# Kernel optimization log

Measured on AMD Instinct MI355X. Metric: run time of the kernel, lower is better.

The kernel has to match this reference:

```python
import jax, jax.numpy as jnp
import numpy as np


def setup_inputs() -> dict:
    key = jax.random.key(0)
    k1, k2, k3, k4 = jax.random.split(key, 4)
    B = 50000    # batch nodes (len(neighbor_lists))
    E = 800000   # total neighbor edges (avg degree 16)
    N = 100000   # unique neighbor embedding rows
    D = 96       # feature dim
    embedding = jax.random.normal(k1, (B * 0 + N, D), dtype=jnp.float32)
    self_feats = jax.random.normal(k2, (B, D), dtype=jnp.float32)
    neighbor_idx = jax.random.randint(k3, (E,), 0, N, dtype=jnp.int64)
    seg_ids = jnp.sort(jax.random.randint(k4, (E,), 0, B, dtype=jnp.int64))
    return {
        "embedding": embedding,
        "self_feats": self_feats,
        "neighbor_idx": neighbor_idx,
        "seg_ids": seg_ids,
    }


def reference(embedding, self_feats, neighbor_idx, seg_ids):
    # Segment-mean aggregation: equivalent to the original's row-normalized
    # dense mask matmul mask.mm(embedding[neighbors_new_index]), but without
    # materializing the [B, n_unique] mask.
    B = self_feats.shape[0]
    gathered = embedding[neighbor_idx]                          # [E, D]
    sums = jax.ops.segment_sum(gathered, seg_ids, num_segments=B)   # [B, D]
    counts = jax.ops.segment_sum(
        jnp.ones(seg_ids.shape, dtype=embedding.dtype), seg_ids, num_segments=B
    )                                                            # [B]
    # every batch node has >=1 neighbor in the original; guard div-by-zero
    feats_1 = sums / jnp.maximum(counts, 1)[:, None]             # neighbor mean
    feats_2 = self_feats - feats_1
    return jnp.concatenate([feats_1, feats_2], axis=1)          # [B, 2D]
```

## Files before the change

### kernel.cpp

```cpp
#include <hip/hip_runtime.h>
#include <stdint.h>

#define DIMS 96
#define VEC 4
#define LANES (DIMS / VEC)
#define SEGS_PER_BLOCK 16
#define THREADS (LANES * SEGS_PER_BLOCK)

__global__ __launch_bounds__(THREADS) void seg_mean_concat_kernel(
    const float* __restrict__ emb,
    const float* __restrict__ self_feats,
    const int*   __restrict__ nidx,
    const int*   __restrict__ seg,
    float* __restrict__ out,
    int B, int E)
{
    __shared__ int bounds[SEGS_PER_BLOCK + 1];

    const int b0 = blockIdx.x * SEGS_PER_BLOCK;
    const int tid = threadIdx.x;

    if (tid <= SEGS_PER_BLOCK) {
        const int v = b0 + tid;
        int lo = 0, hi = E;
        while (lo < hi) {
            int mid = (lo + hi) >> 1;
            if (seg[mid] < v) lo = mid + 1; else hi = mid;
        }
        bounds[tid] = lo;
    }
    __syncthreads();

    const int g    = tid / LANES;
    const int lane = tid - g * LANES;
    const int b    = b0 + g;
    if (b >= B) return;

    const int start = bounds[g];
    const int end   = bounds[g + 1];

    const float4* __restrict__ embv = (const float4*)emb;

    float4 acc = make_float4(0.f, 0.f, 0.f, 0.f);

    int e = start;
    for (; e + 8 <= end; e += 8) {
        const int j0 = nidx[e + 0];
        const int j1 = nidx[e + 1];
        const int j2 = nidx[e + 2];
        const int j3 = nidx[e + 3];
        const int j4 = nidx[e + 4];
        const int j5 = nidx[e + 5];
        const int j6 = nidx[e + 6];
        const int j7 = nidx[e + 7];
        const float4 v0 = embv[(size_t)j0 * LANES + lane];
        const float4 v1 = embv[(size_t)j1 * LANES + lane];
        const float4 v2 = embv[(size_t)j2 * LANES + lane];
        const float4 v3 = embv[(size_t)j3 * LANES + lane];
        const float4 v4 = embv[(size_t)j4 * LANES + lane];
        const float4 v5 = embv[(size_t)j5 * LANES + lane];
        const float4 v6 = embv[(size_t)j6 * LANES + lane];
        const float4 v7 = embv[(size_t)j7 * LANES + lane];
        acc.x += v0.x + v1.x + v2.x + v3.x + v4.x + v5.x + v6.x + v7.x;
        acc.y += v0.y + v1.y + v2.y + v3.y + v4.y + v5.y + v6.y + v7.y;
        acc.z += v0.z + v1.z + v2.z + v3.z + v4.z + v5.z + v6.z + v7.z;
        acc.w += v0.w + v1.w + v2.w + v3.w + v4.w + v5.w + v6.w + v7.w;
    }
    for (; e < end; ++e) {
        const int j = nidx[e];
        const float4 v = embv[(size_t)j * LANES + lane];
        acc.x += v.x; acc.y += v.y; acc.z += v.z; acc.w += v.w;
    }

    const int cnt = end - start;
    const float inv = 1.0f / (float)(cnt > 0 ? cnt : 1);
    float4 mean;
    mean.x = acc.x * inv; mean.y = acc.y * inv;
    mean.z = acc.z * inv; mean.w = acc.w * inv;

    const float4 sf = *(const float4*)(self_feats + (size_t)b * DIMS + lane * VEC);
    float4 diff;
    diff.x = sf.x - mean.x; diff.y = sf.y - mean.y;
    diff.z = sf.z - mean.z; diff.w = sf.w - mean.w;

    float* orow = out + (size_t)b * (2 * DIMS);
    *(float4*)(orow + lane * VEC)        = mean;
    *(float4*)(orow + DIMS + lane * VEC) = diff;
}

extern "C" void kernel_launch(void* const* d_in, const int* in_sizes, int n_in,
                              void* d_out, int out_size, void* d_ws, size_t ws_size,
                              hipStream_t stream) {
    const float* emb        = (const float*)d_in[0];
    const float* self_feats = (const float*)d_in[1];
    const int*   nidx       = (const int*)d_in[2];
    const int*   seg        = (const int*)d_in[3];
    float*       out        = (float*)d_out;

    const int B = in_sizes[1] / DIMS;
    const int E = in_sizes[2];

    const int grid = (B + SEGS_PER_BLOCK - 1) / SEGS_PER_BLOCK;
    hipLaunchKernelGGL(seg_mean_concat_kernel, dim3(grid), dim3(THREADS), 0, stream,
                       emb, self_feats, nidx, seg, out, B, E);
}
```

Measured before the change: 68.78 us.

## Split each segment's edges across two lane groups and stage indices in LDS

Each segment is now handled by two 24-lane groups that take alternating edges, and their partial sums are combined through shared memory. The block's neighbor indices are first copied cooperatively into LDS, so the gather loop reads indices from shared memory instead of global memory. The self-feature load is issued before the gather to overlap it. This aims to raise memory-level parallelism and shorten per-segment latency chains, at the cost of an extra barrier and partial-sum exchange. A barrier placed after an early return could misbehave when B is not a multiple of the block's segment count.

```diff
diff --git a/kernel.cpp b/kernel.cpp
--- a/kernel.cpp
+++ b/kernel.cpp
@@ -4,8 +4,11 @@
 #define DIMS 96
 #define VEC 4
 #define LANES (DIMS / VEC)
-#define SEGS_PER_BLOCK 16
-#define THREADS (LANES * SEGS_PER_BLOCK)
+#define SPLIT 2
+#define GLANES (LANES * SPLIT)
+#define SEGS_PER_BLOCK 8
+#define THREADS (GLANES * SEGS_PER_BLOCK)
+#define IDX_CAP 1024
 
 __global__ __launch_bounds__(THREADS) void seg_mean_concat_kernel(
     const float* __restrict__ emb,
@@ -16,6 +19,8 @@
     int B, int E)
 {
     __shared__ int bounds[SEGS_PER_BLOCK + 1];
+    __shared__ int sidx[IDX_CAP];
+    __shared__ float4 psum[SEGS_PER_BLOCK][LANES];
 
     const int b0 = blockIdx.x * SEGS_PER_BLOCK;
     const int tid = threadIdx.x;
@@ -31,8 +36,18 @@
     }
     __syncthreads();
 
-    const int g    = tid / LANES;
-    const int lane = tid - g * LANES;
+    const int e0    = bounds[0];
+    const int total = bounds[SEGS_PER_BLOCK] - e0;
+    const bool staged = (total <= IDX_CAP);
+    if (staged) {
+        for (int i = tid; i < total; i += THREADS) sidx[i] = nidx[e0 + i];
+    }
+    __syncthreads();
+
+    const int g    = tid / GLANES;
+    const int r    = tid - g * GLANES;
+    const int sub  = r / LANES;
+    const int lane = r - sub * LANES;
     const int b    = b0 + g;
     if (b >= B) return;
 
@@ -41,36 +56,69 @@
 
     const float4* __restrict__ embv = (const float4*)emb;
 
+    float4 sf = make_float4(0.f, 0.f, 0.f, 0.f);
+    if (sub == 0) sf = *(const float4*)(self_feats + (size_t)b * DIMS + lane * VEC);
+
     float4 acc = make_float4(0.f, 0.f, 0.f, 0.f);
 
-    int e = start;
-    for (; e + 8 <= end; e += 8) {
-        const int j0 = nidx[e + 0];
-        const int j1 = nidx[e + 1];
-        const int j2 = nidx[e + 2];
-        const int j3 = nidx[e + 3];
-        const int j4 = nidx[e + 4];
-        const int j5 = nidx[e + 5];
-        const int j6 = nidx[e + 6];
-        const int j7 = nidx[e + 7];
-        const float4 v0 = embv[(size_t)j0 * LANES + lane];
-        const float4 v1 = embv[(size_t)j1 * LANES + lane];
-        const float4 v2 = embv[(size_t)j2 * LANES + lane];
-        const float4 v3 = embv[(size_t)j3 * LANES + lane];
-        const float4 v4 = embv[(size_t)j4 * LANES + lane];
-        const float4 v5 = embv[(size_t)j5 * LANES + lane];
-        const float4 v6 = embv[(size_t)j6 * LANES + lane];
-        const float4 v7 = embv[(size_t)j7 * LANES + lane];
-        acc.x += v0.x + v1.x + v2.x + v3.x + v4.x + v5.x + v6.x + v7.x;
-        acc.y += v0.y + v1.y + v2.y + v3.y + v4.y + v5.y + v6.y + v7.y;
-        acc.z += v0.z + v1.z + v2.z + v3.z + v4.z + v5.z + v6.z + v7.z;
-        acc.w += v0.w + v1.w + v2.w + v3.w + v4.w + v5.w + v6.w + v7.w;
+    if (staged) {
+        const int s1 = end - e0;
+        int e = (start - e0) + sub;
+        for (; e + 7 * SPLIT < s1; e += 8 * SPLIT) {
+            const int j0 = sidx[e + 0 * SPLIT];
+            const int j1 = sidx[e + 1 * SPLIT];
+            const int j2 = sidx[e + 2 * SPLIT];
+            const int j3 = sidx[e + 3 * SPLIT];
+            const int j4 = sidx[e + 4 * SPLIT];
+            const int j5 = sidx[e + 5 * SPLIT];
+            const int j6 = sidx[e + 6 * SPLIT];
+            const int j7 = sidx[e + 7 * SPLIT];
+            const float4 v0 = embv[(size_t)j0 * LANES + lane];
+            const float4 v1 = embv[(size_t)j1 * LANES + lane];
+            const float4 v2 = embv[(size_t)j2 * LANES + lane];
+            const float4 v3 = embv[(size_t)j3 * LANES + lane];
+            const float4 v4 = embv[(size_t)j4 * LANES + lane];
+            const float4 v5 = embv[(size_t)j5 * LANES + lane];
+            const float4 v6 = embv[(size_t)j6 * LANES + lane];
+            const float4 v7 = embv[(size_t)j7 * LANES + lane];
+            acc.x += v0.x + v1.x + v2.x + v3.x + v4.x + v5.x + v6.x + v7.x;
+            acc.y += v0.y + v1.y + v2.y + v3.y + v4.y + v5.y + v6.y + v7.y;
+            acc.z += v0.z + v1.z + v2.z + v3.z + v4.z + v5.z + v6.z + v7.z;
+            acc.w += v0.w + v1.w + v2.w + v3.w + v4.w + v5.w + v6.w + v7.w;
+        }
+        for (; e + 3 * SPLIT < s1; e += 4 * SPLIT) {
+            const int j0 = sidx[e + 0 * SPLIT];
+            const int j1 = sidx[e + 1 * SPLIT];
+            const int j2 = sidx[e + 2 * SPLIT];
+            const int j3 = sidx[e + 3 * SPLIT];
+            const float4 v0 = embv[(size_t)j0 * LANES + lane];
+            const float4 v1 = embv[(size_t)j1 * LANES + lane];
+            const float4 v2 = embv[(size_t)j2 * LANES + lane];
+            const float4 v3 = embv[(size_t)j3 * LANES + lane];
+            acc.x += v0.x + v1.x + v2.x + v3.x;
+            acc.y += v0.y + v1.y + v2.y + v3.y;
+            acc.z += v0.z + v1.z + v2.z + v3.z;
+            acc.w += v0.w + v1.w + v2.w + v3.w;
+        }
+        for (; e < s1; e += SPLIT) {
+            const int j = sidx[e];
+            const float4 v = embv[(size_t)j * LANES + lane];
+            acc.x += v.x; acc.y += v.y; acc.z += v.z; acc.w += v.w;
+        }
+    } else {
+        for (int e = start + sub; e < end; e += SPLIT) {
+            const int j = nidx[e];
+            const float4 v = embv[(size_t)j * LANES + lane];
+            acc.x += v.x; acc.y += v.y; acc.z += v.z; acc.w += v.w;
+        }
     }
-    for (; e < end; ++e) {
-        const int j = nidx[e];
-        const float4 v = embv[(size_t)j * LANES + lane];
-        acc.x += v.x; acc.y += v.y; acc.z += v.z; acc.w += v.w;
-    }
+
+    if (sub == 1) psum[g][lane] = acc;
+    __syncthreads();
+    if (sub != 0) return;
+
+    const float4 p = psum[g][lane];
+    acc.x += p.x; acc.y += p.y; acc.z += p.z; acc.w += p.w;
 
     const int cnt = end - start;
     const float inv = 1.0f / (float)(cnt > 0 ? cnt : 1);
@@ -78,7 +126,6 @@
     mean.x = acc.x * inv; mean.y = acc.y * inv;
     mean.z = acc.z * inv; mean.w = acc.w * inv;
 
-    const float4 sf = *(const float4*)(self_feats + (size_t)b * DIMS + lane * VEC);
     float4 diff;
     diff.x = sf.x - mean.x; diff.y = sf.y - mean.y;
     diff.z = sf.z - mean.z; diff.w = sf.w - mean.w;
```

Result: slower. 83.90 us (+22.0%).

## Precompute segment bounds in separate kernel and drop in-block barrier

Applied to the files above, without the earlier changes.

Segment boundaries are now computed once per node by a separate bounds kernel into workspace, so the main kernel no longer needs the block-level binary search and __syncthreads. If the workspace is too small, each thread falls back to its own binary search. Block size is halved to 8 segments, the self-feature load is hoisted ahead of the gather loop, and the accumulator is split in two with scheduling barriers to group the gather loads. This adds a kernel launch and an extra global round-trip for the bounds.

```diff
diff --git a/kernel.cpp b/kernel.cpp
--- a/kernel.cpp
+++ b/kernel.cpp
@@ -4,44 +4,57 @@
 #define DIMS 96
 #define VEC 4
 #define LANES (DIMS / VEC)
-#define SEGS_PER_BLOCK 16
+#define SEGS_PER_BLOCK 8
 #define THREADS (LANES * SEGS_PER_BLOCK)
+
+
+__global__ __launch_bounds__(256) void bounds_kernel(
+    const int* __restrict__ seg, int* __restrict__ bounds, int B, int E)
+{
+    const int t = blockIdx.x * blockDim.x + threadIdx.x;
+    if (t > B) return;
+    int lo = 0, hi = E;
+    while (lo < hi) {
+        const int mid = (lo + hi) >> 1;
+        if (seg[mid] < t) lo = mid + 1; else hi = mid;
+    }
+    bounds[t] = lo;
+}
 
 __global__ __launch_bounds__(THREADS) void seg_mean_concat_kernel(
     const float* __restrict__ emb,
     const float* __restrict__ self_feats,
     const int*   __restrict__ nidx,
     const int*   __restrict__ seg,
+    const int*   __restrict__ bounds,
     float* __restrict__ out,
     int B, int E)
 {
-    __shared__ int bounds[SEGS_PER_BLOCK + 1];
-
-    const int b0 = blockIdx.x * SEGS_PER_BLOCK;
-    const int tid = threadIdx.x;
-
-    if (tid <= SEGS_PER_BLOCK) {
-        const int v = b0 + tid;
-        int lo = 0, hi = E;
-        while (lo < hi) {
-            int mid = (lo + hi) >> 1;
-            if (seg[mid] < v) lo = mid + 1; else hi = mid;
-        }
-        bounds[tid] = lo;
-    }
-    __syncthreads();
-
+    const int tid  = threadIdx.x;
     const int g    = tid / LANES;
     const int lane = tid - g * LANES;
-    const int b    = b0 + g;
+    const int b    = blockIdx.x * SEGS_PER_BLOCK + g;
     if (b >= B) return;
 
-    const int start = bounds[g];
-    const int end   = bounds[g + 1];
+    int start, end;
+    if (bounds) {
+        start = bounds[b];
+        end   = bounds[b + 1];
+    } else {
+        int lo = 0, hi = E;
+        while (lo < hi) { int m = (lo + hi) >> 1; if (seg[m] < b) lo = m + 1; else hi = m; }
+        start = lo;
+        hi = E;
+        while (lo < hi) { int m = (lo + hi) >> 1; if (seg[m] < b + 1) lo = m + 1; else hi = m; }
+        end = lo;
+    }
 
     const float4* __restrict__ embv = (const float4*)emb;
 
-    float4 acc = make_float4(0.f, 0.f, 0.f, 0.f);
+    const float4 sf = *(const float4*)(self_feats + (size_t)b * DIMS + lane * VEC);
+
+    float4 a0 = make_float4(0.f, 0.f, 0.f, 0.f);
+    float4 a1 = make_float4(0.f, 0.f, 0.f, 0.f);
 
     int e = start;
     for (; e + 8 <= end; e += 8) {
@@ -53,6 +66,7 @@
         const int j5 = nidx[e + 5];
         const int j6 = nidx[e + 6];
         const int j7 = nidx[e + 7];
+        __builtin_amdgcn_sched_group_barrier(0x20 , 8, 0);
         const float4 v0 = embv[(size_t)j0 * LANES + lane];
         const float4 v1 = embv[(size_t)j1 * LANES + lane];
         const float4 v2 = embv[(size_t)j2 * LANES + lane];
@@ -61,24 +75,30 @@
         const float4 v5 = embv[(size_t)j5 * LANES + lane];
         const float4 v6 = embv[(size_t)j6 * LANES + lane];
         const float4 v7 = embv[(size_t)j7 * LANES + lane];
-        acc.x += v0.x + v1.x + v2.x + v3.x + v4.x + v5.x + v6.x + v7.x;
-        acc.y += v0.y + v1.y + v2.y + v3.y + v4.y + v5.y + v6.y + v7.y;
-        acc.z += v0.z + v1.z + v2.z + v3.z + v4.z + v5.z + v6.z + v7.z;
-        acc.w += v0.w + v1.w + v2.w + v3.w + v4.w + v5.w + v6.w + v7.w;
+        __builtin_amdgcn_sched_group_barrier(0x20 , 8, 0);
+        a0.x += v0.x + v2.x + v4.x + v6.x;
+        a0.y += v0.y + v2.y + v4.y + v6.y;
+        a0.z += v0.z + v2.z + v4.z + v6.z;
+        a0.w += v0.w + v2.w + v4.w + v6.w;
+        a1.x += v1.x + v3.x + v5.x + v7.x;
+        a1.y += v1.y + v3.y + v5.y + v7.y;
+        a1.z += v1.z + v3.z + v5.z + v7.z;
+        a1.w += v1.w + v3.w + v5.w + v7.w;
     }
     for (; e < end; ++e) {
         const int j = nidx[e];
         const float4 v = embv[(size_t)j * LANES + lane];
-        acc.x += v.x; acc.y += v.y; acc.z += v.z; acc.w += v.w;
+        a0.x += v.x; a0.y += v.y; a0.z += v.z; a0.w += v.w;
     }
 
     const int cnt = end - start;
     const float inv = 1.0f / (float)(cnt > 0 ? cnt : 1);
     float4 mean;
-    mean.x = acc.x * inv; mean.y = acc.y * inv;
-    mean.z = acc.z * inv; mean.w = acc.w * inv;
+    mean.x = (a0.x + a1.x) * inv;
+    mean.y = (a0.y + a1.y) * inv;
+    mean.z = (a0.z + a1.z) * inv;
+    mean.w = (a0.w + a1.w) * inv;
 
-    const float4 sf = *(const float4*)(self_feats + (size_t)b * DIMS + lane * VEC);
     float4 diff;
     diff.x = sf.x - mean.x; diff.y = sf.y - mean.y;
     diff.z = sf.z - mean.z; diff.w = sf.w - mean.w;
@@ -100,7 +120,15 @@
     const int B = in_sizes[1] / DIMS;
     const int E = in_sizes[2];
 
+    int* bounds = nullptr;
+    if (ws_size >= (size_t)(B + 1) * sizeof(int)) {
+        bounds = (int*)d_ws;
+        const int bgrid = (B + 1 + 255) / 256;
+        hipLaunchKernelGGL(bounds_kernel, dim3(bgrid), dim3(256), 0, stream,
+                           seg, bounds, B, E);
+    }
+
     const int grid = (B + SEGS_PER_BLOCK - 1) / SEGS_PER_BLOCK;
     hipLaunchKernelGGL(seg_mean_concat_kernel, dim3(grid), dim3(THREADS), 0, stream,
-                       emb, self_feats, nidx, seg, out, B, E);
+                       emb, self_feats, nidx, seg, bounds, out, B, E);
 }
```

Result: faster. 62.07 us (-9.7%).
